# Kernel tuning notes

Hardware: AMD Instinct MI355X
Metric: run time of the kernel (lower is better)

## Reference

```python
import jax, jax.numpy as jnp
import numpy as np

B, N, C = 4, 2048, 768
H, QK_R, VP_R = 12, 32, 32  # heads, per-head q/k rank, per-head v rank
HEAD_DIM = 64               # original head_dim -> scale = head_dim ** -0.5


def setup_inputs() -> dict:
    key = jax.random.key(0)
    kx, kq, kk, kv, kp = jax.random.split(key, 5)
    s = lambda fan_in: 1.0 / np.sqrt(fan_in)
    return {
        "x": jax.random.normal(kx, (B, N, C), dtype=jnp.float32),
        "Wq": jax.random.normal(kq, (C, H * QK_R), dtype=jnp.float32) * s(C),
        "Wk": jax.random.normal(kk, (C, H * QK_R), dtype=jnp.float32) * s(C),
        "Wv": jax.random.normal(kv, (C, H * VP_R), dtype=jnp.float32) * s(C),
        "Wp": jax.random.normal(kp, (H * VP_R, C), dtype=jnp.float32) * s(H * VP_R),
    }


def reference(x, Wq, Wk, Wv, Wp):
    b, n, c = x.shape
    scale = HEAD_DIM ** -0.5
    # low-rank projections, split per head: [B, H, N, r]
    q = (x @ Wq).reshape(b, n, H, QK_R).transpose(0, 2, 1, 3)
    k = (x @ Wk).reshape(b, n, H, QK_R).transpose(0, 2, 1, 3)
    v = (x @ Wv).reshape(b, n, H, VP_R).transpose(0, 2, 1, 3)
    attn = jnp.einsum("bhnr,bhmr->bhnm", q, k) * scale  # [B, H, N, N]
    attn = jax.nn.softmax(attn, axis=-1)                 # attn_drop rate 0 -> identity
    out = jnp.einsum("bhnm,bhmr->bhnr", attn, v)        # [B, H, N, VP_R]
    out = out.transpose(0, 2, 1, 3).reshape(b, n, H * VP_R)
    return out @ Wp                                      # proj_drop rate 0 -> identity
```

## Files before the change

kernel.cpp:

```cpp
#include <hip/hip_runtime.h>
#include <hip/hip_bf16.h>
#include <stdint.h>
#include <math.h>

#define B_   4
#define N_   2048
#define C_   768
#define H_   12
#define R_   32
#define M_   (B_ * N_)
#define QKV_ (H_ * R_)

#define QSCALE 0.18033688011112042f

#define KST 40
#define VST 136

typedef __attribute__((ext_vector_type(8))) short    bf16x8;
typedef __attribute__((ext_vector_type(4))) float    f32x4;
typedef __attribute__((ext_vector_type(8))) unsigned short u16x8;
typedef __attribute__((ext_vector_type(4))) _Float16 f16x4;
typedef __attribute__((ext_vector_type(8))) _Float16 f16x8;

#if defined(__has_builtin)
#if __has_builtin(__builtin_amdgcn_exp2f)
#define EXP2F(x) __builtin_amdgcn_exp2f(x)
#else
#define EXP2F(x) exp2f(x)
#endif
#else
#define EXP2F(x) exp2f(x)
#endif

__device__ __forceinline__ short f2bf(float f) {
    union { float f; uint32_t u; } v; v.f = f;
    uint32_t u = v.u;
    uint32_t r = (u + 0x7fffu + ((u >> 16) & 1u)) >> 16;
    return (short)r;
}

__device__ __forceinline__ uint32_t packbf2(float a, float b) {
    __hip_bfloat162 h = __float22bfloat162_rn(float2{a, b});
    uint32_t u; __builtin_memcpy(&u, &h, 4); return u;
}

__device__ __forceinline__ uint32_t packh2(float a, float b) {
    auto h = __builtin_amdgcn_cvt_pkrtz(a, b);
    uint32_t u; __builtin_memcpy(&u, &h, 4); return u;
}

__device__ __forceinline__ void gll16(const short* g, short* l) {
    __builtin_amdgcn_global_load_lds(
        (const __attribute__((address_space(1))) uint32_t*)g,
        (__attribute__((address_space(3))) uint32_t*)l, 16, 0, 0);
}

__global__ __launch_bounds__(256) void prep(
    const float* __restrict__ X,
    const float* __restrict__ Wq, const float* __restrict__ Wk,
    const float* __restrict__ Wv, const float* __restrict__ Wp,
    short* __restrict__ wts, short* __restrict__ wpt, short* __restrict__ Xb) {
    int bid = blockIdx.x;
    if (bid < 288) {
        __shared__ short Ls[64 * 65];
        int z = bid / 72;
        int t = bid - z * 72;
        const float* src; float scl; short* dst; int trt, tct, Psrc, Pdst;
        if (z < 3) {
            trt = t / 6; tct = t - (t / 6) * 6;
            Psrc = 384; Pdst = 768;
            src = (z == 0) ? Wq : (z == 1) ? Wk : Wv;
            scl = (z == 0) ? QSCALE : 1.0f;
            dst = wts + (size_t)z * (QKV_ * C_);
        } else {
            trt = t / 12; tct = t - (t / 12) * 12;
            Psrc = 768; Pdst = 384;
            src = Wp; scl = 1.0f; dst = wpt;
        }
        int r0 = trt * 64, c0 = tct * 64;
        int rr = threadIdx.x >> 2;
        int cc = (threadIdx.x & 3) * 16;
        const float4* s4 = (const float4*)(src + (size_t)(r0 + rr) * Psrc + c0 + cc);
        float4 f0 = s4[0], f1 = s4[1], f2 = s4[2], f3 = s4[3];
        short* lp = &Ls[rr * 65 + cc];
        lp[0]=f2bf(f0.x*scl); lp[1]=f2bf(f0.y*scl); lp[2]=f2bf(f0.z*scl); lp[3]=f2bf(f0.w*scl);
        lp[4]=f2bf(f1.x*scl); lp[5]=f2bf(f1.y*scl); lp[6]=f2bf(f1.z*scl); lp[7]=f2bf(f1.w*scl);
        lp[8]=f2bf(f2.x*scl); lp[9]=f2bf(f2.y*scl); lp[10]=f2bf(f2.z*scl); lp[11]=f2bf(f2.w*scl);
        lp[12]=f2bf(f3.x*scl); lp[13]=f2bf(f3.y*scl); lp[14]=f2bf(f3.z*scl); lp[15]=f2bf(f3.w*scl);
        __syncthreads();
        int jr = threadIdx.x >> 2;
        int seg = (threadIdx.x & 3) * 16;
        u16x8 o0, o1;
        #pragma unroll
        for (int u = 0; u < 8; u++) {
            o0[u] = (unsigned short)Ls[(seg + u) * 65 + jr];
            o1[u] = (unsigned short)Ls[(seg + 8 + u) * 65 + jr];
        }
        short* dp = dst + (size_t)(c0 + jr) * Pdst + r0 + seg;
        *(u16x8*)dp = o0;
        *(u16x8*)(dp + 8) = o1;
    } else {
        size_t i = ((size_t)(bid - 288) * 256 + threadIdx.x) * 8;
        const float4* s4 = (const float4*)(X + i);
        float4 f0 = s4[0], f1 = s4[1];
        u16x8 o;
        o[0]=f2bf(f0.x); o[1]=f2bf(f0.y); o[2]=f2bf(f0.z); o[3]=f2bf(f0.w);
        o[4]=f2bf(f1.x); o[5]=f2bf(f1.y); o[6]=f2bf(f1.z); o[7]=f2bf(f1.w);
        *(u16x8*)(Xb + i) = o;
    }
}

__global__ __launch_bounds__(256, 3) void qkv_gemm(
    const short* __restrict__ Xb, const short* __restrict__ wts,
    short* __restrict__ qkvout) {
    const int mt = blockIdx.x, nt = blockIdx.y;
    const int m0 = mt * 128, j0 = nt * 128;
    const int z = nt / 3;

    __shared__ short smem[2 * 128 * 64];
    short* As = smem;
    short* Bs = smem + 128 * 64;
    short* Tt = smem;

    const int tid = threadIdx.x;
    const int lane = tid & 63, w = tid >> 6;
    const int l16 = lane & 15, quad = lane >> 4;
    const int wm = w & 1, wn = w >> 1;

    const int srow = w * 32 + (lane >> 3);
    const int scol = (((lane & 7) ^ (lane >> 3))) * 8;
    const short* pa = Xb  + (size_t)(m0 + srow) * C_ + scol;
    const short* pb = wts + (size_t)(j0 + srow) * C_ + scol;

    f32x4 acc[4][4] = {};

    for (int k0 = 0; k0 < C_; k0 += 64) {
        __syncthreads();
        #pragma unroll
        for (int j = 0; j < 4; j++) {
            gll16(pa + (size_t)j * 8 * C_ + k0, &As[(w * 32 + j * 8) * 64]);
            gll16(pb + (size_t)j * 8 * C_ + k0, &Bs[(w * 32 + j * 8) * 64]);
        }
        __syncthreads();
        #pragma unroll
        for (int ks = 0; ks < 2; ks++) {
            bf16x8 af[4], bf[4];
            #pragma unroll
            for (int i = 0; i < 4; i++) {
                int ar = wm * 64 + i * 16 + l16;
                af[i] = *(const bf16x8*)&As[ar * 64 + (((ks * 4 + quad) ^ (ar & 7)) * 8)];
                int br = wn * 64 + i * 16 + l16;
                bf[i] = *(const bf16x8*)&Bs[br * 64 + (((ks * 4 + quad) ^ (br & 7)) * 8)];
            }
            #pragma unroll
            for (int i = 0; i < 4; i++)
                #pragma unroll
                for (int c = 0; c < 4; c++)
                    acc[i][c] = __builtin_amdgcn_mfma_f32_16x16x32_bf16(af[i], bf[c], acc[i][c], 0, 0, 0);
        }
    }

    const size_t S = (size_t)B_ * H_ * N_ * R_;
    if (z < 2) {
        #pragma unroll
        for (int c = 0; c < 4; c++) {
            int j = j0 + wn * 64 + c * 16 + l16;
            int zz = j / 384;
            int jz = j - zz * 384;
            int h = jz >> 5, r = jz & 31;
            short* outz = qkvout + (size_t)zz * S;
            #pragma unroll
            for (int i = 0; i < 4; i++) {
                #pragma unroll
                for (int reg = 0; reg < 4; reg++) {
                    int m = m0 + wm * 64 + i * 16 + quad * 4 + reg;
                    int bb = m >> 11, n = m & (N_ - 1);
                    outz[(((size_t)(bb * H_ + h)) * N_ + n) * R_ + r] = f2bf(acc[i][c][reg]);
                }
            }
        }
    } else {
        const int bb = m0 >> 11;
        const int nl0 = m0 & (N_ - 1);
        short* vout = qkvout + 2 * S;
        #pragma unroll
        for (int p = 0; p < 2; p++) {
            __syncthreads();
            if (wn == p) {
                #pragma unroll
                for (int i = 0; i < 4; i++)
                    #pragma unroll
                    for (int c = 0; c < 4; c++) {
                        uint32_t d0 = packh2(acc[i][c][0], acc[i][c][1]);
                        uint32_t d1 = packh2(acc[i][c][2], acc[i][c][3]);
                        uint2 dd = {d0, d1};
                        *(uint2*)&Tt[(c * 16 + l16) * 132 + wm * 64 + i * 16 + quad * 4] = dd;
                    }
            }
            __syncthreads();
            int jr = tid >> 2;
            int seg = (tid & 3) * 32;
            int jz = (nt - 6) * 128 + p * 64 + jr;
            int hh = jz >> 5, rr = jz & 31;
            short* dst = vout + (((size_t)(bb * H_ + hh)) * R_ + rr) * N_ + nl0 + seg;
            #pragma unroll
            for (int q4 = 0; q4 < 4; q4++) {
                u16x8 vv = *(const u16x8*)&Tt[jr * 132 + seg + q4 * 8];
                *(u16x8*)(dst + q4 * 8) = vv;
            }
        }
    }
}

__global__ __launch_bounds__(512, 6) void attn(
    const short* __restrict__ qkv, short* __restrict__ O) {
    const int qt = blockIdx.x, h = blockIdx.y, b = blockIdx.z;
    const size_t S = (size_t)B_ * H_ * N_ * R_;
    const short* Q  = qkv + ((size_t)(b * H_ + h)) * N_ * R_;
    const short* K  = qkv + S + ((size_t)(b * H_ + h)) * N_ * R_;
    const short* Vt = qkv + 2 * S + ((size_t)(b * H_ + h)) * R_ * N_;

    __shared__ short sbuf[2 * 128 * KST + 2 * 32 * VST];
    short* Ksb = sbuf;
    short* Vsb = sbuf + 2 * 128 * KST;

    const int tid = threadIdx.x;
    const int lane = tid & 63, wave = tid >> 6;
    const int wq = wave & 3, wk = wave >> 2;
    const int l16 = lane & 15, quad = lane >> 4;

    bf16x8 aq[2];
    #pragma unroll
    for (int g = 0; g < 2; g++)
        aq[g] = *(const bf16x8*)(Q + (size_t)(qt * 128 + wq * 32 + g * 16 + l16) * R_ + quad * 8);

    f16x8 ones8;
    #pragma unroll
    for (int j = 0; j < 8; j++) ones8[j] = (_Float16)1.0f;

    f32x4 o0T[2] = {}, o1T[2] = {}, lacc[2] = {};

    const int krow = tid >> 2;
    const int kseg = (tid & 3) * 8;
    const short* kgp = K + (size_t)krow * R_ + kseg;
    const int kwoff = krow * KST + kseg;
    const int vrow = tid >> 4;
    const int vcol = (tid & 15) * 8;
    const short* vgp = Vt + (size_t)vrow * N_ + vcol;
    const int vwoff = vrow * VST + vcol;

    {
        u16x8 ka = *(const u16x8*)kgp;
        u16x8 va = *(const u16x8*)vgp;
        *(u16x8*)&Ksb[kwoff] = ka;
        *(u16x8*)&Vsb[vwoff] = va;
    }
    __syncthreads();

    for (int it = 0; it < 16; ++it) {
        const int kt0 = it * 128;
        const int cur = it & 1;
        u16x8 kn, vn;
        if (it < 15) {
            kn = *(const u16x8*)(kgp + (size_t)(kt0 + 128) * R_);
            vn = *(const u16x8*)(vgp + kt0 + 128);
        }

        const short* Kc = &Ksb[cur * 128 * KST];
        const short* Vc = &Vsb[cur * 32 * VST];

        bf16x8 kf[4];
        #pragma unroll
        for (int c = 0; c < 4; c++)
            kf[c] = *(const bf16x8*)&Kc[((wk * 4 + c) * 16 + l16) * KST + quad * 8];

        #pragma unroll
        for (int p = 0; p < 2; p++) {
            const int pp = wk * 2 + p;
            union V8 { struct { f16x4 lo, hi; } h; f16x8 v; };
            V8 v0u, v1u;
            v0u.h.lo = *(const f16x4*)&Vc[l16 * VST + pp * 32 + quad * 4];
            v0u.h.hi = *(const f16x4*)&Vc[l16 * VST + pp * 32 + 16 + quad * 4];
            v1u.h.lo = *(const f16x4*)&Vc[(16 + l16) * VST + pp * 32 + quad * 4];
            v1u.h.hi = *(const f16x4*)&Vc[(16 + l16) * VST + pp * 32 + 16 + quad * 4];
            #pragma unroll
            for (int g = 0; g < 2; g++) {
                f32x4 zz = {};
                f32x4 s0 = __builtin_amdgcn_mfma_f32_16x16x32_bf16(kf[2 * p],     aq[g], zz, 0, 0, 0);
                f32x4 s1 = __builtin_amdgcn_mfma_f32_16x16x32_bf16(kf[2 * p + 1], aq[g], zz, 0, 0, 0);
                union { f16x8 v; uint32_t w[4]; } pu;
                pu.w[0] = packh2(EXP2F(s0[0]), EXP2F(s0[1]));
                pu.w[1] = packh2(EXP2F(s0[2]), EXP2F(s0[3]));
                pu.w[2] = packh2(EXP2F(s1[0]), EXP2F(s1[1]));
                pu.w[3] = packh2(EXP2F(s1[2]), EXP2F(s1[3]));
                o0T[g]  = __builtin_amdgcn_mfma_f32_16x16x32_f16(v0u.v, pu.v, o0T[g], 0, 0, 0);
                o1T[g]  = __builtin_amdgcn_mfma_f32_16x16x32_f16(v1u.v, pu.v, o1T[g], 0, 0, 0);
                lacc[g] = __builtin_amdgcn_mfma_f32_16x16x32_f16(ones8, pu.v, lacc[g], 0, 0, 0);
            }
        }

        if (it < 15) {
            *(u16x8*)&Ksb[(cur ^ 1) * 128 * KST + kwoff] = kn;
            *(u16x8*)&Vsb[(cur ^ 1) * 32 * VST + vwoff]  = vn;
        }
        __syncthreads();
    }

    float* sm = (float*)sbuf;
    if (wk == 1) {
        #pragma unroll
        for (int g = 0; g < 2; g++) {
            int id = (wq * 2 + g) * 64 + lane;
            *(f32x4*)&sm[id * 4]        = o0T[g];
            *(f32x4*)&sm[2048 + id * 4] = o1T[g];
            sm[4096 + id] = lacc[g][0];
        }
    }
    __syncthreads();
    if (wk == 0) {
        #pragma unroll
        for (int g = 0; g < 2; g++) {
            int id = (wq * 2 + g) * 64 + lane;
            f32x4 p0 = *(const f32x4*)&sm[id * 4];
            f32x4 p1 = *(const f32x4*)&sm[2048 + id * 4];
            float pl = sm[4096 + id];
            f32x4 a0 = o0T[g] + p0;
            f32x4 a1 = o1T[g] + p1;
            float inv = 1.0f / (lacc[g][0] + pl);
            int n = qt * 128 + wq * 32 + g * 16 + l16;
            size_t base = ((size_t)b * N_ + n) * QKV_ + h * R_;
            uint32_t a0w = packbf2(a0[0] * inv, a0[1] * inv);
            uint32_t a1w = packbf2(a0[2] * inv, a0[3] * inv);
            uint2 s0 = {a0w, a1w};
            *(uint2*)&O[base + quad * 4] = s0;
            uint32_t b0w = packbf2(a1[0] * inv, a1[1] * inv);
            uint32_t b1w = packbf2(a1[2] * inv, a1[3] * inv);
            uint2 s1 = {b0w, b1w};
            *(uint2*)&O[base + 16 + quad * 4] = s1;
        }
    }
}

__global__ __launch_bounds__(256, 3) void out_gemm(
    const short* __restrict__ Ob, const short* __restrict__ wpt,
    float* __restrict__ out) {
    const int mt = blockIdx.x, nt = blockIdx.y;
    const int m0 = mt * 128, j0 = nt * 64;

    __shared__ short As[128 * 64];
    __shared__ short Bs[64 * 64];

    const int tid = threadIdx.x;
    const int lane = tid & 63, w = tid >> 6;
    const int l16 = lane & 15, quad = lane >> 4;

    const int sarow = w * 32 + (lane >> 3);
    const int sbrow = w * 16 + (lane >> 3);
    const int scol = (((lane & 7) ^ (lane >> 3))) * 8;
    const short* pa = Ob  + (size_t)(m0 + sarow) * QKV_ + scol;
    const short* pb = wpt + (size_t)(j0 + sbrow) * QKV_ + scol;

    f32x4 acc[2][4] = {};

    for (int k0 = 0; k0 < QKV_; k0 += 64) {
        __syncthreads();
        #pragma unroll
        for (int j = 0; j < 4; j++)
            gll16(pa + (size_t)j * 8 * QKV_ + k0, &As[(w * 32 + j * 8) * 64]);
        #pragma unroll
        for (int j = 0; j < 2; j++)
            gll16(pb + (size_t)j * 8 * QKV_ + k0, &Bs[(w * 16 + j * 8) * 64]);
        __syncthreads();
        #pragma unroll
        for (int ks = 0; ks < 2; ks++) {
            bf16x8 af[2], bf[4];
            #pragma unroll
            for (int i = 0; i < 2; i++) {
                int ar = w * 32 + i * 16 + l16;
                af[i] = *(const bf16x8*)&As[ar * 64 + (((ks * 4 + quad) ^ (ar & 7)) * 8)];
            }
            #pragma unroll
            for (int c = 0; c < 4; c++) {
                int br = c * 16 + l16;
                bf[c] = *(const bf16x8*)&Bs[br * 64 + (((ks * 4 + quad) ^ (br & 7)) * 8)];
            }
            #pragma unroll
            for (int i = 0; i < 2; i++)
                #pragma unroll
                for (int c = 0; c < 4; c++)
                    acc[i][c] = __builtin_amdgcn_mfma_f32_16x16x32_bf16(af[i], bf[c], acc[i][c], 0, 0, 0);
        }
    }

    #pragma unroll
    for (int i = 0; i < 2; i++)
        #pragma unroll
        for (int c = 0; c < 4; c++)
            #pragma unroll
            for (int reg = 0; reg < 4; reg++) {
                int m = m0 + w * 32 + i * 16 + quad * 4 + reg;
                out[(size_t)m * C_ + j0 + c * 16 + l16] = acc[i][c][reg];
            }
}

extern "C" void kernel_launch(void* const* d_in, const int* in_sizes, int n_in,
                              void* d_out, int out_size, void* d_ws, size_t ws_size,
                              hipStream_t stream) {
    const float* x  = (const float*)d_in[0];
    const float* Wq = (const float*)d_in[1];
    const float* Wk = (const float*)d_in[2];
    const float* Wv = (const float*)d_in[3];
    const float* Wp = (const float*)d_in[4];
    float* out = (float*)d_out;

    short* ws16 = (short*)d_ws;
    short* wts  = ws16;
    short* wpt  = wts + (size_t)3 * QKV_ * C_;
    short* qkv  = wpt + (size_t)QKV_ * C_;
    short* Obuf = qkv + (size_t)3 * B_ * H_ * N_ * R_;
    short* Xb   = Obuf + (size_t)B_ * N_ * QKV_;

    prep<<<dim3(288 + 3072), 256, 0, stream>>>(x, Wq, Wk, Wv, Wp, wts, wpt, Xb);
    qkv_gemm<<<dim3(M_ / 128, (3 * QKV_) / 128), 256, 0, stream>>>(Xb, wts, qkv);
    attn<<<dim3(N_ / 128, H_, B_), 512, 0, stream>>>(qkv, Obuf);
    out_gemm<<<dim3(M_ / 128, C_ / 64), 256, 0, stream>>>(Obuf, wpt, out);
}
```

Before: 150.1 us.

## Halve attention query tile and split keys across four wave groups

The attention kernel now handles 64 queries per block instead of 128. The 8 waves are arranged as 2 query groups by 4 key groups, where before they were 4 by 2, and the grid doubles along the query dimension. Each wave processes 32 keys per tile instead of 64, and the cross-wave reduction now sums three partials through shared memory. This gives more blocks and fewer registers per wave, allowing higher occupancy (launch bounds raised to 8). The cost is twice as many K/V tile loads per output and more reduction work at the end.

```diff
diff --git a/kernel.cpp b/kernel.cpp
--- a/kernel.cpp
+++ b/kernel.cpp
@@ -212,7 +212,7 @@
     }
 }
 
-__global__ __launch_bounds__(512, 6) void attn(
+__global__ __launch_bounds__(512, 8) void attn(
     const short* __restrict__ qkv, short* __restrict__ O) {
     const int qt = blockIdx.x, h = blockIdx.y, b = blockIdx.z;
     const size_t S = (size_t)B_ * H_ * N_ * R_;
@@ -226,13 +226,13 @@
 
     const int tid = threadIdx.x;
     const int lane = tid & 63, wave = tid >> 6;
-    const int wq = wave & 3, wk = wave >> 2;
+    const int wq = wave & 1, wk = wave >> 1;
     const int l16 = lane & 15, quad = lane >> 4;
 
     bf16x8 aq[2];
     #pragma unroll
     for (int g = 0; g < 2; g++)
-        aq[g] = *(const bf16x8*)(Q + (size_t)(qt * 128 + wq * 32 + g * 16 + l16) * R_ + quad * 8);
+        aq[g] = *(const bf16x8*)(Q + (size_t)(qt * 64 + wq * 32 + g * 16 + l16) * R_ + quad * 8);
 
     f16x8 ones8;
     #pragma unroll
@@ -269,34 +269,31 @@
         const short* Kc = &Ksb[cur * 128 * KST];
         const short* Vc = &Vsb[cur * 32 * VST];
 
-        bf16x8 kf[4];
-        #pragma unroll
-        for (int c = 0; c < 4; c++)
-            kf[c] = *(const bf16x8*)&Kc[((wk * 4 + c) * 16 + l16) * KST + quad * 8];
-
-        #pragma unroll
-        for (int p = 0; p < 2; p++) {
-            const int pp = wk * 2 + p;
-            union V8 { struct { f16x4 lo, hi; } h; f16x8 v; };
-            V8 v0u, v1u;
-            v0u.h.lo = *(const f16x4*)&Vc[l16 * VST + pp * 32 + quad * 4];
-            v0u.h.hi = *(const f16x4*)&Vc[l16 * VST + pp * 32 + 16 + quad * 4];
-            v1u.h.lo = *(const f16x4*)&Vc[(16 + l16) * VST + pp * 32 + quad * 4];
-            v1u.h.hi = *(const f16x4*)&Vc[(16 + l16) * VST + pp * 32 + 16 + quad * 4];
-            #pragma unroll
-            for (int g = 0; g < 2; g++) {
-                f32x4 zz = {};
-                f32x4 s0 = __builtin_amdgcn_mfma_f32_16x16x32_bf16(kf[2 * p],     aq[g], zz, 0, 0, 0);
-                f32x4 s1 = __builtin_amdgcn_mfma_f32_16x16x32_bf16(kf[2 * p + 1], aq[g], zz, 0, 0, 0);
-                union { f16x8 v; uint32_t w[4]; } pu;
-                pu.w[0] = packh2(EXP2F(s0[0]), EXP2F(s0[1]));
-                pu.w[1] = packh2(EXP2F(s0[2]), EXP2F(s0[3]));
-                pu.w[2] = packh2(EXP2F(s1[0]), EXP2F(s1[1]));
-                pu.w[3] = packh2(EXP2F(s1[2]), EXP2F(s1[3]));
-                o0T[g]  = __builtin_amdgcn_mfma_f32_16x16x32_f16(v0u.v, pu.v, o0T[g], 0, 0, 0);
-                o1T[g]  = __builtin_amdgcn_mfma_f32_16x16x32_f16(v1u.v, pu.v, o1T[g], 0, 0, 0);
-                lacc[g] = __builtin_amdgcn_mfma_f32_16x16x32_f16(ones8, pu.v, lacc[g], 0, 0, 0);
-            }
+        bf16x8 kf[2];
+        #pragma unroll
+        for (int c = 0; c < 2; c++)
+            kf[c] = *(const bf16x8*)&Kc[((wk * 2 + c) * 16 + l16) * KST + quad * 8];
+
+        union V8 { struct { f16x4 lo, hi; } h; f16x8 v; };
+        V8 v0u, v1u;
+        v0u.h.lo = *(const f16x4*)&Vc[l16 * VST + wk * 32 + quad * 4];
+        v0u.h.hi = *(const f16x4*)&Vc[l16 * VST + wk * 32 + 16 + quad * 4];
+        v1u.h.lo = *(const f16x4*)&Vc[(16 + l16) * VST + wk * 32 + quad * 4];
+        v1u.h.hi = *(const f16x4*)&Vc[(16 + l16) * VST + wk * 32 + 16 + quad * 4];
+
+        #pragma unroll
+        for (int g = 0; g < 2; g++) {
+            f32x4 zz = {};
+            f32x4 s0 = __builtin_amdgcn_mfma_f32_16x16x32_bf16(kf[0], aq[g], zz, 0, 0, 0);
+            f32x4 s1 = __builtin_amdgcn_mfma_f32_16x16x32_bf16(kf[1], aq[g], zz, 0, 0, 0);
+            union { f16x8 v; uint32_t w[4]; } pu;
+            pu.w[0] = packh2(EXP2F(s0[0]), EXP2F(s0[1]));
+            pu.w[1] = packh2(EXP2F(s0[2]), EXP2F(s0[3]));
+            pu.w[2] = packh2(EXP2F(s1[0]), EXP2F(s1[1]));
+            pu.w[3] = packh2(EXP2F(s1[2]), EXP2F(s1[3]));
+            o0T[g]  = __builtin_amdgcn_mfma_f32_16x16x32_f16(v0u.v, pu.v, o0T[g], 0, 0, 0);
+            o1T[g]  = __builtin_amdgcn_mfma_f32_16x16x32_f16(v1u.v, pu.v, o1T[g], 0, 0, 0);
+            lacc[g] = __builtin_amdgcn_mfma_f32_16x16x32_f16(ones8, pu.v, lacc[g], 0, 0, 0);
         }
 
         if (it < 15) {
@@ -307,27 +304,31 @@
     }
 
     float* sm = (float*)sbuf;
-    if (wk == 1) {
+    if (wk > 0) {
         #pragma unroll
         for (int g = 0; g < 2; g++) {
-            int id = (wq * 2 + g) * 64 + lane;
+            int id = (((wk - 1) * 2 + wq) * 2 + g) * 64 + lane;
             *(f32x4*)&sm[id * 4]        = o0T[g];
-            *(f32x4*)&sm[2048 + id * 4] = o1T[g];
-            sm[4096 + id] = lacc[g][0];
+            *(f32x4*)&sm[3072 + id * 4] = o1T[g];
+            sm[6144 + id] = lacc[g][0];
         }
     }
     __syncthreads();
     if (wk == 0) {
         #pragma unroll
         for (int g = 0; g < 2; g++) {
-            int id = (wq * 2 + g) * 64 + lane;
-            f32x4 p0 = *(const f32x4*)&sm[id * 4];
-            f32x4 p1 = *(const f32x4*)&sm[2048 + id * 4];
-            float pl = sm[4096 + id];
-            f32x4 a0 = o0T[g] + p0;
-            f32x4 a1 = o1T[g] + p1;
-            float inv = 1.0f / (lacc[g][0] + pl);
-            int n = qt * 128 + wq * 32 + g * 16 + l16;
+            f32x4 a0 = o0T[g];
+            f32x4 a1 = o1T[g];
+            float l = lacc[g][0];
+            #pragma unroll
+            for (int w2 = 0; w2 < 3; w2++) {
+                int id = ((w2 * 2 + wq) * 2 + g) * 64 + lane;
+                a0 += *(const f32x4*)&sm[id * 4];
+                a1 += *(const f32x4*)&sm[3072 + id * 4];
+                l  += sm[6144 + id];
+            }
+            float inv = 1.0f / l;
+            int n = qt * 64 + wq * 32 + g * 16 + l16;
             size_t base = ((size_t)b * N_ + n) * QKV_ + h * R_;
             uint32_t a0w = packbf2(a0[0] * inv, a0[1] * inv);
             uint32_t a1w = packbf2(a0[2] * inv, a0[3] * inv);
@@ -422,6 +423,6 @@
 
     prep<<<dim3(288 + 3072), 256, 0, stream>>>(x, Wq, Wk, Wv, Wp, wts, wpt, Xb);
     qkv_gemm<<<dim3(M_ / 128, (3 * QKV_) / 128), 256, 0, stream>>>(Xb, wts, qkv);
-    attn<<<dim3(N_ / 128, H_, B_), 512, 0, stream>>>(qkv, Obuf);
+    attn<<<dim3(N_ / 64, H_, B_), 512, 0, stream>>>(qkv, Obuf);
     out_gemm<<<dim3(M_ / 128, C_ / 64), 256, 0, stream>>>(Obuf, wpt, out);
 }
```

New measurement: 156.6 us. +4.4%, slower.
